# Kernel tuning notes

Measured on AMD Instinct MI355X. Metric: run time of the kernel, lower is better.

## Reference

```python
import jax, jax.numpy as jnp
import numpy as np
import math

D_MODEL = 1024
N_HEADS = 8
D_FF = 4 * D_MODEL
EPS = 1e-5


def layer_norm(x, g, b):
    mu = jnp.mean(x, axis=-1, keepdims=True)
    var = jnp.mean(jnp.square(x - mu), axis=-1, keepdims=True)
    return (x - mu) / jnp.sqrt(var + EPS) * g + b


def setup_inputs() -> dict:
    key = jax.random.key(0)
    ks = jax.random.split(key, 8)
    B, S = 1, 4096
    x = jax.random.normal(ks[0], (B, S, D_MODEL), dtype=jnp.float32)
    # linear params (stored as [in, out]); init scale ~ 1/sqrt(fan_in)
    qkv_w = jax.random.normal(ks[1], (D_MODEL, 3 * D_MODEL), dtype=jnp.float32) * (1.0 / math.sqrt(D_MODEL))
    qkv_b = jnp.zeros((3 * D_MODEL,), dtype=jnp.float32)
    w1 = jax.random.normal(ks[2], (D_MODEL, D_FF), dtype=jnp.float32) * (1.0 / math.sqrt(D_MODEL))
    b1 = jnp.zeros((D_FF,), dtype=jnp.float32)
    w2 = jax.random.normal(ks[3], (D_FF, D_MODEL), dtype=jnp.float32) * (1.0 / math.sqrt(D_FF))
    b2 = jnp.zeros((D_MODEL,), dtype=jnp.float32)
    ln1_g = jnp.ones((D_MODEL,), dtype=jnp.float32)
    ln1_b = jnp.zeros((D_MODEL,), dtype=jnp.float32)
    ln2_g = jnp.ones((D_MODEL,), dtype=jnp.float32)
    ln2_b = jnp.zeros((D_MODEL,), dtype=jnp.float32)
    return {"x": x, "ln1_g": ln1_g, "ln1_b": ln1_b, "qkv_w": qkv_w, "qkv_b": qkv_b,
            "ln2_g": ln2_g, "ln2_b": ln2_b, "w1": w1, "b1": b1, "w2": w2, "b2": b2}


def reference(x, ln1_g, ln1_b, qkv_w, qkv_b, ln2_g, ln2_b, w1, b1, w2, b2):
    B, S, D = x.shape
    hd = D // N_HEADS
    scaler = math.sqrt(hd)

    h = layer_norm(x, ln1_g, ln1_b)                       # [B,S,D]
    qkv = h @ qkv_w + qkv_b                               # [B,S,3D]
    q, k, v = jnp.split(qkv, 3, axis=-1)
    # b s (h d) -> b h s d
    def split_heads(t):
        return t.reshape(B, S, N_HEADS, hd).transpose(0, 2, 1, 3)
    q, k, v = split_heads(q), split_heads(k), split_heads(v)
    scores = jnp.einsum('bhqd,bhkd->bhqk', q, k) / scaler  # [B,H,S,S] materialized, as in source
    attn = jax.nn.softmax(scores, axis=-1)
    heads = jnp.einsum('bhqk,bhkd->bhqd', attn, v)        # [B,H,S,hd]
    attn_score = heads.transpose(0, 2, 1, 3).reshape(B, S, D)  # b h t d -> b t (h d)
    # NOTE: source returns attn_score (the proj Linear output is discarded)
    h = attn_score + h                                     # residual with ln1 output
    h = layer_norm(h, ln2_g, ln2_b)
    h = jax.nn.gelu(h @ w1 + b1, approximate=False) @ w2 + b2  # no final residual
    return h
```

## Files before the change

### kernel.cpp

```cpp
#include <hip/hip_runtime.h>
#include <stdint.h>


typedef __bf16 bf16;
typedef __attribute__((ext_vector_type(8))) __bf16 bf16x8;
typedef __attribute__((ext_vector_type(4))) __bf16 bf16x4;
typedef __attribute__((ext_vector_type(4))) float f32x4;

#define DEV static __device__ __forceinline__

#define QSCALE 0.12751741687f

DEV void gload_lds16(const void* gsrc, void* ldst) {
  typedef const __attribute__((address_space(1))) uint32_t gq_t;
  typedef __attribute__((address_space(3))) uint32_t lq_t;
  __builtin_amdgcn_global_load_lds((gq_t*)(uintptr_t)gsrc, (lq_t*)(uintptr_t)ldst,
                                   16, 0, 0);
}

DEV f32x4 mfma16(bf16x8 a, bf16x8 b, f32x4 c) {
  return __builtin_amdgcn_mfma_f32_16x16x32_bf16(a, b, c, 0, 0, 0);
}

__global__ __launch_bounds__(256) void ln1_kernel(
    const float* __restrict__ x, const float* __restrict__ gw,
    const float* __restrict__ bw, bf16* __restrict__ out) {
  int row = blockIdx.x, t = threadIdx.x;
  const float* xr = x + (size_t)row * 1024;
  f32x4 v = *(const f32x4*)(xr + t * 4);
  float s = v[0] + v[1] + v[2] + v[3];
  float s2 = v[0] * v[0] + v[1] * v[1] + v[2] * v[2] + v[3] * v[3];
#pragma unroll
  for (int off = 1; off < 64; off <<= 1) {
    s += __shfl_xor(s, off);
    s2 += __shfl_xor(s2, off);
  }
  __shared__ float red[8];
  if ((t & 63) == 0) { red[t >> 6] = s; red[4 + (t >> 6)] = s2; }
  __syncthreads();
  s = red[0] + red[1] + red[2] + red[3];
  s2 = red[4] + red[5] + red[6] + red[7];
  float mu = s * (1.f / 1024.f);
  float rstd = rsqrtf(s2 * (1.f / 1024.f) - mu * mu + 1e-5f);
  f32x4 gv = *(const f32x4*)(gw + t * 4);
  f32x4 bv = *(const f32x4*)(bw + t * 4);
  bf16x4 o;
#pragma unroll
  for (int j = 0; j < 4; j++) o[j] = (bf16)((v[j] - mu) * rstd * gv[j] + bv[j]);
  *(bf16x4*)(out + (size_t)row * 1024 + t * 4) = o;
}

__global__ __launch_bounds__(256) void resid_ln2_kernel(
    const float* __restrict__ O0, const float* __restrict__ O1,
    const float* __restrict__ lbuf, const bf16* __restrict__ h,
    const float* __restrict__ gw, const float* __restrict__ bw,
    bf16* __restrict__ out) {
  int row = blockIdx.x, t = threadIdx.x;
  int head = t >> 5;
  float l = lbuf[head * 4096 + row] + lbuf[(8 + head) * 4096 + row];
  float rl = 1.0f / l;
  f32x4 a0 = *(const f32x4*)(O0 + (size_t)row * 1024 + t * 4);
  f32x4 a1 = *(const f32x4*)(O1 + (size_t)row * 1024 + t * 4);
  bf16x4 hv = *(const bf16x4*)(h + (size_t)row * 1024 + t * 4);
  float vv[4];
#pragma unroll
  for (int j = 0; j < 4; j++) vv[j] = (a0[j] + a1[j]) * rl + (float)hv[j];
  float s = vv[0] + vv[1] + vv[2] + vv[3];
  float s2 = vv[0] * vv[0] + vv[1] * vv[1] + vv[2] * vv[2] + vv[3] * vv[3];
#pragma unroll
  for (int off = 1; off < 64; off <<= 1) {
    s += __shfl_xor(s, off);
    s2 += __shfl_xor(s2, off);
  }
  __shared__ float red[8];
  if ((t & 63) == 0) { red[t >> 6] = s; red[4 + (t >> 6)] = s2; }
  __syncthreads();
  s = red[0] + red[1] + red[2] + red[3];
  s2 = red[4] + red[5] + red[6] + red[7];
  float mu = s * (1.f / 1024.f);
  float rstd = rsqrtf(s2 * (1.f / 1024.f) - mu * mu + 1e-5f);
  f32x4 gv = *(const f32x4*)(gw + t * 4);
  f32x4 bv = *(const f32x4*)(bw + t * 4);
  bf16x4 o;
#pragma unroll
  for (int j = 0; j < 4; j++) o[j] = (bf16)((vv[j] - mu) * rstd * gv[j] + bv[j]);
  *(bf16x4*)(out + (size_t)row * 1024 + t * 4) = o;
}

__global__ __launch_bounds__(256) void transpose_f32_bf16(
    const float* __restrict__ in, bf16* __restrict__ out, int R, int C) {
  __shared__ float tile[32][33];
  int c0 = blockIdx.x * 32, r0 = blockIdx.y * 32;
  int tx = threadIdx.x & 31, ty = threadIdx.x >> 5;
#pragma unroll
  for (int j = 0; j < 4; j++)
    tile[ty + 8 * j][tx] = in[(size_t)(r0 + ty + 8 * j) * C + c0 + tx];
  __syncthreads();
#pragma unroll
  for (int j = 0; j < 4; j++)
    out[(size_t)(c0 + ty + 8 * j) * R + r0 + tx] = (bf16)tile[tx][ty + 8 * j];
}

template <int EPILOG>
__global__ __launch_bounds__(512) void gemm8_kernel(
    const bf16* __restrict__ A, const bf16* __restrict__ Bt,
    const float* __restrict__ bias, bf16* __restrict__ Cout,
    bf16* __restrict__ Vout, int M, int N, int K) {
  __shared__ bf16 sA[256 * 64];
  __shared__ bf16 sB[128 * 64];
  int nwg = gridDim.x * gridDim.y;
  int bid = blockIdx.y * gridDim.x + blockIdx.x;
  int swz = (bid & 7) * (nwg >> 3) + (bid >> 3);
  int bx = swz % gridDim.x, by = swz / gridDim.x;
  int m0 = by * 256, n0 = bx * 128;
  int tid = threadIdx.x;
  int wave = tid >> 6, lane = tid & 63;
  int lr = lane & 15, lg = lane >> 4;
  int wr = (wave >> 1) * 64, wc = (wave & 1) * 64;

  f32x4 acc[4][4] = {};

  int srow = tid >> 3;
  int scol = (tid & 7) * 8;
  const bf16* Abase = A + (size_t)(m0 + srow) * K + scol;
  const bf16* Bbase = Bt + (size_t)(n0 + srow) * K + scol;

  for (int kt = 0; kt < K; kt += 64) {
#pragma unroll
    for (int i = 0; i < 4; i++)
      gload_lds16(Abase + (size_t)(i * 64) * K + kt,
                  (char*)sA + i * 8192 + wave * 1024);
#pragma unroll
    for (int i = 0; i < 2; i++)
      gload_lds16(Bbase + (size_t)(i * 64) * K + kt,
                  (char*)sB + i * 8192 + wave * 1024);
    __syncthreads();
    bf16x8 af[4][2], bfv[4][2];
#pragma unroll
    for (int m = 0; m < 4; m++)
#pragma unroll
      for (int kk = 0; kk < 2; kk++)
        af[m][kk] = *(const bf16x8*)&sA[(wr + m * 16 + lr) * 64 + kk * 32 + lg * 8];
#pragma unroll
    for (int n = 0; n < 4; n++)
#pragma unroll
      for (int kk = 0; kk < 2; kk++)
        bfv[n][kk] = *(const bf16x8*)&sB[(wc + n * 16 + lr) * 64 + kk * 32 + lg * 8];
#pragma unroll
    for (int kk = 0; kk < 2; kk++)
#pragma unroll
      for (int m = 0; m < 4; m++)
#pragma unroll
        for (int n = 0; n < 4; n++)
          acc[m][n] = mfma16(af[m][kk], bfv[n][kk], acc[m][n]);
    __syncthreads();
  }

#pragma unroll
  for (int n = 0; n < 4; n++) {
    int col = n0 + wc + n * 16 + lr;
    float bs = bias[col];
#pragma unroll
    for (int m = 0; m < 4; m++) {
      int row0 = m0 + wr + m * 16 + lg * 4;
      if constexpr (EPILOG == 3) {
        if (col >= 2048) {
          bf16x4 pk;
#pragma unroll
          for (int r = 0; r < 4; r++) pk[r] = (bf16)(acc[m][n][r] + bs);
          *(bf16x4*)(Vout + (size_t)(col - 2048) * 4096 + row0) = pk;
          continue;
        }
      }
#pragma unroll
      for (int r = 0; r < 4; r++) {
        float v = acc[m][n][r] + bs;
        if constexpr (EPILOG == 1) {
          float u = v + 0.044715f * v * v * v;
          float e = __builtin_amdgcn_exp2f(-2.3021144f * u);
          v = v / (1.0f + e);
        }
        if constexpr (EPILOG == 3) { if (col < 1024) v *= QSCALE; }
        Cout[(size_t)(row0 + r) * N + col] = (bf16)v;
      }
    }
  }
}

__global__ __launch_bounds__(256) void gemm_ffn2_kernel(
    const bf16* __restrict__ A, const bf16* __restrict__ Bt,
    const float* __restrict__ bias, float* __restrict__ Cout,
    int M, int N, int K) {
  __shared__ bf16 sA[64 * 64];
  __shared__ bf16 sB[128 * 64];
  int nwg = gridDim.x * gridDim.y;
  int bid = blockIdx.y * gridDim.x + blockIdx.x;
  int swz = (bid & 7) * (nwg >> 3) + (bid >> 3);
  int bx = swz % gridDim.x, by = swz / gridDim.x;
  int m0 = by * 64, n0 = bx * 128;
  int tid = threadIdx.x;
  int wave = tid >> 6, lane = tid & 63;
  int lr = lane & 15, lg = lane >> 4;
  int wr = (wave >> 1) * 32, wc = (wave & 1) * 64;

  f32x4 acc[2][4] = {};

  int srow = tid >> 3;
  int scol = (tid & 7) * 8;
  const bf16* Abase = A + (size_t)(m0 + srow) * K + scol;
  const bf16* Bbase = Bt + (size_t)(n0 + srow) * K + scol;

  for (int kt = 0; kt < K; kt += 64) {
#pragma unroll
    for (int i = 0; i < 2; i++)
      gload_lds16(Abase + (size_t)(i * 32) * K + kt,
                  (char*)sA + i * 4096 + wave * 1024);
#pragma unroll
    for (int i = 0; i < 4; i++)
      gload_lds16(Bbase + (size_t)(i * 32) * K + kt,
                  (char*)sB + i * 4096 + wave * 1024);
    __syncthreads();
    bf16x8 af[2][2], bfv[4][2];
#pragma unroll
    for (int m = 0; m < 2; m++)
#pragma unroll
      for (int kk = 0; kk < 2; kk++)
        af[m][kk] = *(const bf16x8*)&sA[(wr + m * 16 + lr) * 64 + kk * 32 + lg * 8];
#pragma unroll
    for (int n = 0; n < 4; n++)
#pragma unroll
      for (int kk = 0; kk < 2; kk++)
        bfv[n][kk] = *(const bf16x8*)&sB[(wc + n * 16 + lr) * 64 + kk * 32 + lg * 8];
#pragma unroll
    for (int kk = 0; kk < 2; kk++)
#pragma unroll
      for (int m = 0; m < 2; m++)
#pragma unroll
        for (int n = 0; n < 4; n++)
          acc[m][n] = mfma16(af[m][kk], bfv[n][kk], acc[m][n]);
    __syncthreads();
  }

#pragma unroll
  for (int n = 0; n < 4; n++) {
    int col = n0 + wc + n * 16 + lr;
    float bs = bias[col];
#pragma unroll
    for (int m = 0; m < 2; m++) {
#pragma unroll
      for (int r = 0; r < 4; r++) {
        int row = m0 + wr + m * 16 + lg * 4 + r;
        Cout[(size_t)row * N + col] = acc[m][n][r] + bs;
      }
    }
  }
}

__global__ __launch_bounds__(256) void attn_kernel(
    const bf16* __restrict__ qkv, const bf16* __restrict__ vt,
    float* __restrict__ opart, float* __restrict__ lbuf) {
  constexpr int S = 4096, C3 = 3072;
  __shared__ bf16 sK[64 * 128];
  __shared__ bf16 sV[128 * 64];
  __shared__ bf16 sP[4 * 32 * 64];
  int hh = blockIdx.y;
  int q0 = blockIdx.x * 128;
  int z = blockIdx.z;
  int kv_begin = z * (S / 2), kv_end = kv_begin + (S / 2);
  float* obuf = opart + (size_t)z * 4096 * 1024;
  int tid = threadIdx.x, wave = tid >> 6, lane = tid & 63;
  int lr = lane & 15, lg = lane >> 4;

  bf16x8 qf[2][4];
#pragma unroll
  for (int qs = 0; qs < 2; qs++) {
    const bf16* qrow =
        qkv + (size_t)(q0 + wave * 32 + qs * 16 + lr) * C3 + hh * 128 + lg * 8;
#pragma unroll
    for (int kk = 0; kk < 4; kk++) qf[qs][kk] = *(const bf16x8*)(qrow + kk * 32);
  }
  f32x4 o[2][8] = {};
  float lsum[2] = {0.f, 0.f};

  const int krow_s = tid >> 4;
  const int kcb = (tid & 15) * 16;
  const int scbK = kcb ^ ((krow_s & 7) << 4);
  const int vrow_s = tid >> 3;
  const int vcb = (tid & 7) * 16;
  const int scbV = vcb ^ ((vrow_s & 7) << 4);

  const bf16* kbase = qkv + 1024 + hh * 128 + scbK / 2;
  const bf16* vbase = vt + (size_t)(hh * 128 + vrow_s) * S + scbV / 2;

  for (int kv0 = kv_begin; kv0 < kv_end; kv0 += 64) {
#pragma unroll
    for (int i = 0; i < 4; i++)
      gload_lds16(kbase + (size_t)(kv0 + i * 16 + krow_s) * C3,
                  (char*)sK + i * 4096 + wave * 1024);
#pragma unroll
    for (int i = 0; i < 4; i++)
      gload_lds16(vbase + (size_t)(i * 32) * S + kv0,
                  (char*)sV + i * 4096 + wave * 1024);
    __syncthreads();

    char* pw = (char*)sP + wave * 4096;

#pragma unroll
    for (int nf = 0; nf < 4; nf++) {
      f32x4 sc0 = {0.f, 0.f, 0.f, 0.f}, sc1 = sc0;
      __builtin_amdgcn_s_setprio(1);
#pragma unroll
      for (int kk = 0; kk < 4; kk++) {
        int krow = nf * 16 + lr;
        int db = (kk * 64 + lg * 16) ^ ((krow & 7) << 4);
        bf16x8 kf = *(const bf16x8*)((const char*)sK + krow * 256 + db);
        sc0 = mfma16(kf, qf[0][kk], sc0);
        sc1 = mfma16(kf, qf[1][kk], sc1);
      }
      __builtin_amdgcn_s_setprio(0);
      f32x4 scs[2] = {sc0, sc1};
#pragma unroll
      for (int qs = 0; qs < 2; qs++) {
        float p0 = __builtin_amdgcn_exp2f(scs[qs][0]);
        float p1 = __builtin_amdgcn_exp2f(scs[qs][1]);
        float p2 = __builtin_amdgcn_exp2f(scs[qs][2]);
        float p3 = __builtin_amdgcn_exp2f(scs[qs][3]);
        lsum[qs] += (p0 + p1) + (p2 + p3);
        bf16x4 pk;
        pk[0] = (bf16)p0; pk[1] = (bf16)p1; pk[2] = (bf16)p2; pk[3] = (bf16)p3;
        *(bf16x4*)(pw + (qs * 16 + lr) * 128 +
                   ((nf * 32 + lg * 8) ^ ((lr & 7) << 4))) = pk;
      }
    }

    bf16x8 pa[2][2];
#pragma unroll
    for (int qs = 0; qs < 2; qs++)
#pragma unroll
      for (int kk = 0; kk < 2; kk++) {
        int db = (kk * 64 + lg * 16) ^ ((lr & 7) << 4);
        pa[qs][kk] = *(const bf16x8*)(pw + (qs * 16 + lr) * 128 + db);
      }
    __builtin_amdgcn_s_setprio(1);
#pragma unroll
    for (int df = 0; df < 8; df++) {
#pragma unroll
      for (int kk = 0; kk < 2; kk++) {
        int vrow = df * 16 + lr;
        int db = (kk * 64 + lg * 16) ^ ((vrow & 7) << 4);
        bf16x8 vf = *(const bf16x8*)((const char*)sV + vrow * 128 + db);
        o[0][df] = mfma16(pa[0][kk], vf, o[0][df]);
        o[1][df] = mfma16(pa[1][kk], vf, o[1][df]);
      }
    }
    __builtin_amdgcn_s_setprio(0);
    __syncthreads();
  }

#pragma unroll
  for (int qs = 0; qs < 2; qs++) {
    float ls = lsum[qs];
    ls += __shfl_xor(ls, 16);
    ls += __shfl_xor(ls, 32);
    if (lg == 0)
      lbuf[(size_t)(z * 8 + hh) * 4096 + q0 + wave * 32 + qs * 16 + lr] = ls;
#pragma unroll
    for (int df = 0; df < 8; df++) {
      int col = hh * 128 + df * 16 + lr;
#pragma unroll
      for (int r = 0; r < 4; r++) {
        int row = q0 + wave * 32 + qs * 16 + lg * 4 + r;
        obuf[(size_t)row * 1024 + col] = o[qs][df][r];
      }
    }
  }
}

extern "C" void kernel_launch(void* const* d_in, const int* in_sizes, int n_in,
                              void* d_out, int out_size, void* d_ws, size_t ws_size,
                              hipStream_t stream) {
  const float* x     = (const float*)d_in[0];
  const float* ln1_g = (const float*)d_in[1];
  const float* ln1_b = (const float*)d_in[2];
  const float* qkv_w = (const float*)d_in[3];
  const float* qkv_b = (const float*)d_in[4];
  const float* ln2_g = (const float*)d_in[5];
  const float* ln2_b = (const float*)d_in[6];
  const float* w1    = (const float*)d_in[7];
  const float* b1    = (const float*)d_in[8];
  const float* w2    = (const float*)d_in[9];
  const float* b2    = (const float*)d_in[10];

  char* ws = (char*)d_ws;
  const size_t MB = 1ull << 20;
  bf16*  h    = (bf16*)(ws + 0);
  bf16*  qkv  = (bf16*)(ws + 8 * MB);
  bf16*  h2   = (bf16*)(ws + 8 * MB);
  bf16*  w1T  = (bf16*)(ws + 16 * MB);
  bf16*  w2T  = (bf16*)(ws + 24 * MB);
  bf16*  vt   = (bf16*)(ws + 32 * MB);
  float* Op   = (float*)(ws + 40 * MB);
  bf16*  ffn1 = (bf16*)(ws + 40 * MB);
  float* lbuf = (float*)(ws + 72 * MB);
  bf16*  wTq  = (bf16*)(ws + 72 * MB + 256 * 1024);
  float* outp = (float*)d_out;

  ln1_kernel<<<4096, 256, 0, stream>>>(x, ln1_g, ln1_b, h);
  transpose_f32_bf16<<<dim3(3072 / 32, 1024 / 32), 256, 0, stream>>>(qkv_w, wTq, 1024, 3072);
  gemm8_kernel<3><<<dim3(3072 / 128, 4096 / 256), 512, 0, stream>>>(
      h, wTq, qkv_b, qkv, vt, 4096, 3072, 1024);
  attn_kernel<<<dim3(32, 8, 2), 256, 0, stream>>>(qkv, vt, Op, lbuf);
  transpose_f32_bf16<<<dim3(4096 / 32, 1024 / 32), 256, 0, stream>>>(w1, w1T, 1024, 4096);
  transpose_f32_bf16<<<dim3(1024 / 32, 4096 / 32), 256, 0, stream>>>(w2, w2T, 4096, 1024);
  resid_ln2_kernel<<<4096, 256, 0, stream>>>(Op, Op + 4096ull * 1024, lbuf, h,
                                             ln2_g, ln2_b, h2);
  gemm8_kernel<1><<<dim3(4096 / 128, 4096 / 256), 512, 0, stream>>>(
      h2, w1T, b1, ffn1, nullptr, 4096, 4096, 1024);
  gemm_ffn2_kernel<<<dim3(1024 / 128, 4096 / 64), 256, 0, stream>>>(
      ffn1, w2T, b2, outp, 4096, 1024, 4096);
}
```

Measured before the change: 276.4 us.

## Split attention KV four ways with bf16 partials and prefetch GEMM tiles

The attention kernel now splits the key/value range into four chunks instead of two, doubling the grid to raise occupancy, and writes the partial outputs as bf16 rather than fp32 to cut write and read traffic. The residual+LN2 kernel sums the four partials. Both GEMM kernels now issue the next K-tile's global-to-LDS loads before the MFMA loop runs, using a single buffer with an extra barrier in gemm8 and a double buffer in the FFN2 GEMM, so loads overlap compute. Storing partials in bf16 loses some precision, and the single-buffer prefetch adds a barrier per iteration.

```diff
diff --git a/kernel.cpp b/kernel.cpp
--- a/kernel.cpp
+++ b/kernel.cpp
@@ -51,20 +51,26 @@
 }
 
 __global__ __launch_bounds__(256) void resid_ln2_kernel(
-    const float* __restrict__ O0, const float* __restrict__ O1,
-    const float* __restrict__ lbuf, const bf16* __restrict__ h,
-    const float* __restrict__ gw, const float* __restrict__ bw,
-    bf16* __restrict__ out) {
+    const bf16* __restrict__ Op, const float* __restrict__ lbuf,
+    const bf16* __restrict__ h, const float* __restrict__ gw,
+    const float* __restrict__ bw, bf16* __restrict__ out) {
   int row = blockIdx.x, t = threadIdx.x;
   int head = t >> 5;
-  float l = lbuf[head * 4096 + row] + lbuf[(8 + head) * 4096 + row];
+  float l = 0.f;
+  float acc[4] = {0.f, 0.f, 0.f, 0.f};
+#pragma unroll
+  for (int z = 0; z < 4; z++) {
+    l += lbuf[(size_t)(z * 8 + head) * 4096 + row];
+    bf16x4 ov = *(const bf16x4*)(Op + (size_t)z * 4096 * 1024 +
+                                 (size_t)row * 1024 + t * 4);
+#pragma unroll
+    for (int j = 0; j < 4; j++) acc[j] += (float)ov[j];
+  }
   float rl = 1.0f / l;
-  f32x4 a0 = *(const f32x4*)(O0 + (size_t)row * 1024 + t * 4);
-  f32x4 a1 = *(const f32x4*)(O1 + (size_t)row * 1024 + t * 4);
   bf16x4 hv = *(const bf16x4*)(h + (size_t)row * 1024 + t * 4);
   float vv[4];
 #pragma unroll
-  for (int j = 0; j < 4; j++) vv[j] = (a0[j] + a1[j]) * rl + (float)hv[j];
+  for (int j = 0; j < 4; j++) vv[j] = acc[j] * rl + (float)hv[j];
   float s = vv[0] + vv[1] + vv[2] + vv[3];
   float s2 = vv[0] * vv[0] + vv[1] * vv[1] + vv[2] * vv[2] + vv[3] * vv[3];
 #pragma unroll
@@ -125,7 +131,7 @@
   const bf16* Abase = A + (size_t)(m0 + srow) * K + scol;
   const bf16* Bbase = Bt + (size_t)(n0 + srow) * K + scol;
 
-  for (int kt = 0; kt < K; kt += 64) {
+  auto stage = [&](int kt) {
 #pragma unroll
     for (int i = 0; i < 4; i++)
       gload_lds16(Abase + (size_t)(i * 64) * K + kt,
@@ -134,6 +140,10 @@
     for (int i = 0; i < 2; i++)
       gload_lds16(Bbase + (size_t)(i * 64) * K + kt,
                   (char*)sB + i * 8192 + wave * 1024);
+  };
+
+  stage(0);
+  for (int kt = 0; kt < K; kt += 64) {
     __syncthreads();
     bf16x8 af[4][2], bfv[4][2];
 #pragma unroll
@@ -146,6 +156,9 @@
 #pragma unroll
       for (int kk = 0; kk < 2; kk++)
         bfv[n][kk] = *(const bf16x8*)&sB[(wc + n * 16 + lr) * 64 + kk * 32 + lg * 8];
+    __syncthreads();
+    if (kt + 64 < K) stage(kt + 64);
+    __builtin_amdgcn_sched_barrier(0);
 #pragma unroll
     for (int kk = 0; kk < 2; kk++)
 #pragma unroll
@@ -153,7 +166,6 @@
 #pragma unroll
         for (int n = 0; n < 4; n++)
           acc[m][n] = mfma16(af[m][kk], bfv[n][kk], acc[m][n]);
-    __syncthreads();
   }
 
 #pragma unroll
@@ -191,8 +203,8 @@
     const bf16* __restrict__ A, const bf16* __restrict__ Bt,
     const float* __restrict__ bias, float* __restrict__ Cout,
     int M, int N, int K) {
-  __shared__ bf16 sA[64 * 64];
-  __shared__ bf16 sB[128 * 64];
+  __shared__ bf16 sA[2][64 * 64];
+  __shared__ bf16 sB[2][128 * 64];
   int nwg = gridDim.x * gridDim.y;
   int bid = blockIdx.y * gridDim.x + blockIdx.x;
   int swz = (bid & 7) * (nwg >> 3) + (bid >> 3);
@@ -210,27 +222,35 @@
   const bf16* Abase = A + (size_t)(m0 + srow) * K + scol;
   const bf16* Bbase = Bt + (size_t)(n0 + srow) * K + scol;
 
-  for (int kt = 0; kt < K; kt += 64) {
+  auto stage = [&](int b, int kt) {
 #pragma unroll
     for (int i = 0; i < 2; i++)
       gload_lds16(Abase + (size_t)(i * 32) * K + kt,
-                  (char*)sA + i * 4096 + wave * 1024);
+                  (char*)sA[b] + i * 4096 + wave * 1024);
 #pragma unroll
     for (int i = 0; i < 4; i++)
       gload_lds16(Bbase + (size_t)(i * 32) * K + kt,
-                  (char*)sB + i * 4096 + wave * 1024);
-    __syncthreads();
+                  (char*)sB[b] + i * 4096 + wave * 1024);
+  };
+
+  stage(0, 0);
+  __syncthreads();
+  int cur = 0;
+  for (int kt = 0; kt < K; kt += 64) {
+    if (kt + 64 < K) stage(cur ^ 1, kt + 64);
     bf16x8 af[2][2], bfv[4][2];
 #pragma unroll
     for (int m = 0; m < 2; m++)
 #pragma unroll
       for (int kk = 0; kk < 2; kk++)
-        af[m][kk] = *(const bf16x8*)&sA[(wr + m * 16 + lr) * 64 + kk * 32 + lg * 8];
+        af[m][kk] =
+            *(const bf16x8*)&sA[cur][(wr + m * 16 + lr) * 64 + kk * 32 + lg * 8];
 #pragma unroll
     for (int n = 0; n < 4; n++)
 #pragma unroll
       for (int kk = 0; kk < 2; kk++)
-        bfv[n][kk] = *(const bf16x8*)&sB[(wc + n * 16 + lr) * 64 + kk * 32 + lg * 8];
+        bfv[n][kk] =
+            *(const bf16x8*)&sB[cur][(wc + n * 16 + lr) * 64 + kk * 32 + lg * 8];
 #pragma unroll
     for (int kk = 0; kk < 2; kk++)
 #pragma unroll
@@ -239,6 +259,7 @@
         for (int n = 0; n < 4; n++)
           acc[m][n] = mfma16(af[m][kk], bfv[n][kk], acc[m][n]);
     __syncthreads();
+    cur ^= 1;
   }
 
 #pragma unroll
@@ -258,7 +279,7 @@
 
 __global__ __launch_bounds__(256) void attn_kernel(
     const bf16* __restrict__ qkv, const bf16* __restrict__ vt,
-    float* __restrict__ opart, float* __restrict__ lbuf) {
+    bf16* __restrict__ opart, float* __restrict__ lbuf) {
   constexpr int S = 4096, C3 = 3072;
   __shared__ bf16 sK[64 * 128];
   __shared__ bf16 sV[128 * 64];
@@ -266,8 +287,8 @@
   int hh = blockIdx.y;
   int q0 = blockIdx.x * 128;
   int z = blockIdx.z;
-  int kv_begin = z * (S / 2), kv_end = kv_begin + (S / 2);
-  float* obuf = opart + (size_t)z * 4096 * 1024;
+  int kv_begin = z * (S / 4), kv_end = kv_begin + (S / 4);
+  bf16* obuf = opart + (size_t)z * 4096 * 1024;
   int tid = threadIdx.x, wave = tid >> 6, lane = tid & 63;
   int lr = lane & 15, lg = lane >> 4;
 
@@ -370,7 +391,7 @@
 #pragma unroll
       for (int r = 0; r < 4; r++) {
         int row = q0 + wave * 32 + qs * 16 + lg * 4 + r;
-        obuf[(size_t)row * 1024 + col] = o[qs][df][r];
+        obuf[(size_t)row * 1024 + col] = (bf16)o[qs][df][r];
       }
     }
   }
@@ -399,21 +420,20 @@
   bf16*  w1T  = (bf16*)(ws + 16 * MB);
   bf16*  w2T  = (bf16*)(ws + 24 * MB);
   bf16*  vt   = (bf16*)(ws + 32 * MB);
-  float* Op   = (float*)(ws + 40 * MB);
+  bf16*  Op   = (bf16*)(ws + 40 * MB);
   bf16*  ffn1 = (bf16*)(ws + 40 * MB);
   float* lbuf = (float*)(ws + 72 * MB);
-  bf16*  wTq  = (bf16*)(ws + 72 * MB + 256 * 1024);
+  bf16*  wTq  = (bf16*)(ws + 72 * MB + 512 * 1024);
   float* outp = (float*)d_out;
 
   ln1_kernel<<<4096, 256, 0, stream>>>(x, ln1_g, ln1_b, h);
   transpose_f32_bf16<<<dim3(3072 / 32, 1024 / 32), 256, 0, stream>>>(qkv_w, wTq, 1024, 3072);
   gemm8_kernel<3><<<dim3(3072 / 128, 4096 / 256), 512, 0, stream>>>(
       h, wTq, qkv_b, qkv, vt, 4096, 3072, 1024);
-  attn_kernel<<<dim3(32, 8, 2), 256, 0, stream>>>(qkv, vt, Op, lbuf);
+  attn_kernel<<<dim3(32, 8, 4), 256, 0, stream>>>(qkv, vt, Op, lbuf);
   transpose_f32_bf16<<<dim3(4096 / 32, 1024 / 32), 256, 0, stream>>>(w1, w1T, 1024, 4096);
   transpose_f32_bf16<<<dim3(1024 / 32, 4096 / 32), 256, 0, stream>>>(w2, w2T, 4096, 1024);
-  resid_ln2_kernel<<<4096, 256, 0, stream>>>(Op, Op + 4096ull * 1024, lbuf, h,
-                                             ln2_g, ln2_b, h2);
+  resid_ln2_kernel<<<4096, 256, 0, stream>>>(Op, lbuf, h, ln2_g, ln2_b, h2);
   gemm8_kernel<1><<<dim3(4096 / 128, 4096 / 256), 512, 0, stream>>>(
       h2, w1T, b1, ffn1, nullptr, 4096, 4096, 1024);
   gemm_ffn2_kernel<<<dim3(1024 / 128, 4096 / 64), 256, 0, stream>>>(
```

After: 296.7 us. 7.4% more time.
